# Performance work log

Hardware: AMD Instinct MI355X
Metric: run time of the kernel (lower is better)

Reference implementation:

```python
import jax, jax.numpy as jnp
import numpy as np

N, E = 100000, 1000000
IN_F, HID, OUT, K = 64, 64, 32, 3


def setup_inputs() -> dict:
    key = jax.random.key(0)
    ks = jax.random.split(key, 8)
    s = 0.05
    return {
        "features": jax.random.normal(ks[0], (N, IN_F), dtype=jnp.float32),
        "src": jax.random.randint(ks[1], (E,), 0, N),
        "dst": jax.random.randint(ks[2], (E,), 0, N),
        "n_nodes": N,
        "W1": jax.random.normal(ks[3], (K * IN_F, HID), jnp.float32) * s,
        "b1": jnp.zeros((HID,), jnp.float32),
        "W2": jax.random.normal(ks[4], (K * HID, HID), jnp.float32) * s,
        "b2": jnp.zeros((HID,), jnp.float32),
        "Wm1": jax.random.normal(ks[5], (HID, HID), jnp.float32) * s,
        "bm1": jnp.zeros((HID,), jnp.float32),
        "Wm2": jax.random.normal(ks[6], (HID, OUT), jnp.float32) * s,
        "bm2": jnp.zeros((OUT,), jnp.float32),
    }


def _cheb_conv(x, src, dst, dinv, W, b, n_nodes, k=K):
    # DGL ChebConv with lambda_max = 2 (re_norm = 2/lambda_max = 1).
    def prop(h):  # D^{-1/2} A D^{-1/2} h via edge gather/scatter
        m = (h * dinv)[src]                                   # [E, F]
        agg = jax.ops.segment_sum(m, dst, num_segments=n_nodes)
        return agg * dinv

    X0 = x
    Xs = [X0]
    X1 = -prop(X0)                 # -re_norm*L h + (re_norm-1)*X0, re_norm=1
    Xs.append(X1)
    for _ in range(2, k):
        Xi = -2.0 * prop(X1) - X0  # Chebyshev recursion
        Xs.append(Xi)
        X0, X1 = X1, Xi
    return jnp.concatenate(Xs, axis=1) @ W + b  # Linear(k*F_in -> F_out)


def reference(features, src, dst, n_nodes, W1, b1, W2, b2, Wm1, bm1, Wm2, bm2):
    deg = jax.ops.segment_sum(
        jnp.ones((src.shape[0],), dtype=features.dtype), dst, num_segments=n_nodes
    )
    dinv = (jnp.clip(deg, 1.0, None) ** -0.5)[:, None]  # in-degree^{-1/2}
    x = jax.nn.relu(_cheb_conv(features, src, dst, dinv, W1, b1, n_nodes))
    x = jax.nn.relu(_cheb_conv(x, src, dst, dinv, W2, b2, n_nodes))
    return jax.nn.relu(x @ Wm1 + bm1) @ Wm2 + bm2
```

## Files before the change

kernel.cpp:

```cpp
#include <hip/hip_runtime.h>


typedef unsigned short ushort_t;
typedef __attribute__((ext_vector_type(8))) short v8s;
typedef __attribute__((ext_vector_type(4))) float v4f;

__device__ inline ushort_t f2bf(float f) {
    unsigned u = __float_as_uint(f);
    return (ushort_t)((u + 0x7FFFu + ((u >> 16) & 1u)) >> 16);
}
__device__ inline float bf2f(ushort_t h) {
    return __uint_as_float(((unsigned)h) << 16);
}

#define BSH 9
#define BSZ (1 << BSH)
#define CHUNK 4096

__global__ void k_wprep(const float* __restrict__ W1, const float* __restrict__ W2,
                        const float* __restrict__ Wm1, const float* __restrict__ Wm2,
                        ushort_t* __restrict__ W1t, ushort_t* __restrict__ W2t,
                        ushort_t* __restrict__ Wm1t, ushort_t* __restrict__ Wm2t,
                        int* __restrict__ gbase, int NB) {
    int i = blockIdx.x * 256 + threadIdx.x;
    if (i < 12288) { int k = i >> 6, n = i & 63; W1t[n * 192 + k] = f2bf(W1[i]); return; }
    i -= 12288;
    if (i < 12288) { int k = i >> 6, n = i & 63; W2t[n * 192 + k] = f2bf(W2[i]); return; }
    i -= 12288;
    if (i < 4096) { int k = i >> 6, n = i & 63; Wm1t[n * 64 + k] = f2bf(Wm1[i]); return; }
    i -= 4096;
    if (i < 2048) { int k = i >> 5, n = i & 31; Wm2t[n * 64 + k] = f2bf(Wm2[i]); return; }
    i -= 2048;
    if (i < NB) gbase[i] = 0;
}


__global__ __launch_bounds__(256) void k_bhist(const int* __restrict__ dst,
                                               int* __restrict__ gbase, int E, int NB) {
    __shared__ int h[1024];
    for (int i = threadIdx.x; i < NB; i += 256) h[i] = 0;
    __syncthreads();
    for (int i = blockIdx.x * blockDim.x + threadIdx.x; i < E; i += gridDim.x * blockDim.x)
        atomicAdd(&h[dst[i] >> BSH], 1);
    __syncthreads();
    for (int i = threadIdx.x; i < NB; i += 256)
        if (h[i]) atomicAdd(&gbase[i], h[i]);
}

__global__ void k_bscan(int* __restrict__ gbase, int* __restrict__ gcur, int NB) {
    __shared__ int sh[1024];
    int t = threadIdx.x;
    int v = (t < NB) ? gbase[t] : 0;
    sh[t] = v;
    __syncthreads();
    for (int off = 1; off < 1024; off <<= 1) {
        int u = 0;
        if (t >= off) u = sh[t - off];
        __syncthreads();
        sh[t] += u;
        __syncthreads();
    }
    if (t < NB) {
        int excl = sh[t] - v;
        gbase[t] = excl;
        gcur[t] = excl;
    }
}

__global__ __launch_bounds__(256) void k_bucket2(
    const int* __restrict__ src, const int* __restrict__ dst,
    int* __restrict__ gcur, int2* __restrict__ eb, int E, int NB) {
    __shared__ int ls[CHUNK];
    __shared__ int ld[CHUNK];
    __shared__ int hist[1024];
    __shared__ int bbase[1024];
    int t = threadIdx.x;
    int base = blockIdx.x * CHUNK;
    int count = E - base;
    if (count > CHUNK) count = CHUNK;
    for (int i = t; i < NB; i += 256) hist[i] = 0;
    __syncthreads();
    for (int i = t; i < count; i += 256) {
        int s = src[base + i];
        int d = dst[base + i];
        ls[i] = s;
        ld[i] = d;
        atomicAdd(&hist[d >> BSH], 1);
    }
    __syncthreads();
    for (int b = t; b < NB; b += 256) {
        int c = hist[b];
        bbase[b] = c ? atomicAdd(&gcur[b], c) : 0;
        hist[b] = 0;
    }
    __syncthreads();
    for (int i = t; i < count; i += 256) {
        int d = ld[i];
        int b = d >> BSH;
        int off = atomicAdd(&hist[b], 1);
        eb[bbase[b] + off] = make_int2(ls[i], d);
    }
}

__global__ __launch_bounds__(256) void k_local(
    const int2* __restrict__ eb, const int* __restrict__ gbase,
    int* __restrict__ col, int* __restrict__ row_ptr,
    float* __restrict__ dinv, int N, int E, int NB) {
    __shared__ int cnt[BSZ];
    __shared__ int tsum[256];
    int t = threadIdx.x;
    int b = blockIdx.x;
    int d0 = b << BSH;
    cnt[2 * t] = 0;
    cnt[2 * t + 1] = 0;
    __syncthreads();
    int beg = gbase[b];
    int end = (b + 1 < NB) ? gbase[b + 1] : E;
    for (int i = beg + t; i < end; i += 256)
        atomicAdd(&cnt[eb[i].y - d0], 1);
    __syncthreads();
    int c0 = cnt[2 * t], c1 = cnt[2 * t + 1];
    int mysum = c0 + c1;
    tsum[t] = mysum;
    __syncthreads();
    for (int off = 1; off < 256; off <<= 1) {
        int u = 0;
        if (t >= off) u = tsum[t - off];
        __syncthreads();
        tsum[t] += u;
        __syncthreads();
    }
    int rbase = beg + tsum[t] - mysum;
    int d = d0 + 2 * t;
    if (d < N) {
        row_ptr[d] = rbase;
        dinv[d] = rsqrtf(fmaxf((float)c0, 1.0f));
    }
    if (d + 1 < N) {
        row_ptr[d + 1] = rbase + c0;
        dinv[d + 1] = rsqrtf(fmaxf((float)c1, 1.0f));
    }
    cnt[2 * t] = rbase;
    cnt[2 * t + 1] = rbase + c0;
    __syncthreads();
    for (int i = beg + t; i < end; i += 256) {
        int2 e = eb[i];
        int p = atomicAdd(&cnt[e.y - d0], 1);
        col[p] = e.x;
    }
    if (b == NB - 1 && t == 0) row_ptr[N] = E;
}

__global__ void k_tobf16(const float4* __restrict__ X, const float* __restrict__ dinv,
                         ushort4* __restrict__ Y, int n4) {
    int i = blockIdx.x * blockDim.x + threadIdx.x;
    if (i < n4) {
        float s = dinv[i >> 4];
        float4 v = X[i];
        ushort4 o;
        o.x = f2bf(v.x * s); o.y = f2bf(v.y * s); o.z = f2bf(v.z * s); o.w = f2bf(v.w * s);
        Y[i] = o;
    }
}

template <int MODE>
__global__ __launch_bounds__(256) void k_prop(
    const ushort_t* __restrict__ Xb, const int* __restrict__ rp,
    const int* __restrict__ col, const float* __restrict__ dinv,
    const ushort_t* __restrict__ X0b, ushort_t* __restrict__ OUTB, int N) {
    int wid = (blockIdx.x * blockDim.x + threadIdx.x) >> 6;
    int lane = threadIdx.x & 63;
    if (wid >= N) return;
    int g = lane >> 4;
    int fl = (lane & 15) * 4;
    int beg = rp[wid], end = rp[wid + 1];
    float4 a0 = make_float4(0.f, 0.f, 0.f, 0.f);
    float4 a1 = make_float4(0.f, 0.f, 0.f, 0.f);
    int e = beg + g;
    for (; e + 4 < end; e += 8) {
        int s0 = col[e], s1 = col[e + 4];
        ushort4 u0 = *(const ushort4*)&Xb[(size_t)s0 * 64 + fl];
        ushort4 u1 = *(const ushort4*)&Xb[(size_t)s1 * 64 + fl];
        a0.x += bf2f(u0.x); a0.y += bf2f(u0.y); a0.z += bf2f(u0.z); a0.w += bf2f(u0.w);
        a1.x += bf2f(u1.x); a1.y += bf2f(u1.y); a1.z += bf2f(u1.z); a1.w += bf2f(u1.w);
    }
    if (e < end) {
        int s0 = col[e];
        ushort4 u0 = *(const ushort4*)&Xb[(size_t)s0 * 64 + fl];
        a0.x += bf2f(u0.x); a0.y += bf2f(u0.y); a0.z += bf2f(u0.z); a0.w += bf2f(u0.w);
    }
    float4 acc;
    acc.x = a0.x + a1.x;
    acc.y = a0.y + a1.y;
    acc.z = a0.z + a1.z;
    acc.w = a0.w + a1.w;
    acc.x += __shfl_xor(acc.x, 16);
    acc.y += __shfl_xor(acc.y, 16);
    acc.z += __shfl_xor(acc.z, 16);
    acc.w += __shfl_xor(acc.w, 16);
    acc.x += __shfl_xor(acc.x, 32);
    acc.y += __shfl_xor(acc.y, 32);
    acc.z += __shfl_xor(acc.z, 32);
    acc.w += __shfl_xor(acc.w, 32);
    if (g == 0) {
        float di = dinv[wid];
        ushort4 ob;
        if (MODE == 1) {
            float m = -di * di;
            ob.x = f2bf(m * acc.x);
            ob.y = f2bf(m * acc.y);
            ob.z = f2bf(m * acc.z);
            ob.w = f2bf(m * acc.w);
        } else {
            ushort4 x0u = *(const ushort4*)&X0b[(size_t)wid * 64 + fl];
            float m = -2.0f * di;
            float rd = 1.0f / di;
            ob.x = f2bf(fmaf(m, acc.x, -rd * bf2f(x0u.x)));
            ob.y = f2bf(fmaf(m, acc.y, -rd * bf2f(x0u.y)));
            ob.z = f2bf(fmaf(m, acc.z, -rd * bf2f(x0u.z)));
            ob.w = f2bf(fmaf(m, acc.w, -rd * bf2f(x0u.w)));
        }
        *(ushort4*)&OUTB[(size_t)wid * 64 + fl] = ob;
    }
}

template <bool SCALE_OUT>
__global__ __launch_bounds__(256, 6) void k_cheb_mfma(
    const ushort_t* __restrict__ X0, const ushort_t* __restrict__ X1,
    const ushort_t* __restrict__ X2, const float* __restrict__ dinv,
    const ushort_t* __restrict__ Wt, const float* __restrict__ b,
    ushort_t* __restrict__ Yb, int N) {
    int wave = threadIdx.x >> 6, lane = threadIdx.x & 63;
    int n16 = lane & 15, q = lane >> 4;
    int node0 = blockIdx.x * 64;
    int arow = node0 + wave * 16 + n16;
    const ushort_t* Xc[3] = {X0, X1, X2};

    v8s av[6];
#pragma unroll
    for (int ks = 0; ks < 6; ks++) {
        int c = ks >> 1;
        int kk = (ks & 1) * 32 + q * 8;
        av[ks] = (v8s){0, 0, 0, 0, 0, 0, 0, 0};
        if (arow < N) av[ks] = *(const v8s*)&Xc[c][(size_t)arow * 64 + kk];
    }

    v4f acc_s[4], acc_u[4];
#pragma unroll
    for (int t = 0; t < 4; t++) {
        acc_s[t] = (v4f){0.f, 0.f, 0.f, 0.f};
        acc_u[t] = (v4f){0.f, 0.f, 0.f, 0.f};
    }
#pragma unroll
    for (int ks = 0; ks < 6; ks++) {
        int c = ks >> 1;
#pragma unroll
        for (int t = 0; t < 4; t++) {
            v8s bv = *(const v8s*)&Wt[(size_t)(t * 16 + n16) * 192 + ks * 32 + q * 8];
            if (c < 2)
                acc_s[t] = __builtin_amdgcn_mfma_f32_16x16x32_bf16(av[ks], bv, acc_s[t], 0, 0, 0);
            else
                acc_u[t] = __builtin_amdgcn_mfma_f32_16x16x32_bf16(av[ks], bv, acc_u[t], 0, 0, 0);
        }
    }
    int rbase = node0 + wave * 16 + q * 4;
#pragma unroll
    for (int r = 0; r < 4; r++) {
        int row = rbase + r;
        if (row < N) {
            float dv = dinv[row];
            float rd = 1.0f / dv;
            float s = SCALE_OUT ? dv : 1.0f;
#pragma unroll
            for (int t = 0; t < 4; t++) {
                float y = fmaf(rd, acc_s[t][r], acc_u[t][r]) + b[t * 16 + n16];
                y = fmaxf(y, 0.0f);
                Yb[(size_t)row * 64 + t * 16 + n16] = f2bf(s * y);
            }
        }
    }
}

__global__ __launch_bounds__(256, 6) void k_cheb_mlp(
    const ushort_t* __restrict__ X0, const ushort_t* __restrict__ X1,
    const ushort_t* __restrict__ X2, const float* __restrict__ dinv,
    const ushort_t* __restrict__ Wt, const float* __restrict__ b,
    const ushort_t* __restrict__ Wm1t, const float* __restrict__ bm1,
    const ushort_t* __restrict__ Wm2t, const float* __restrict__ bm2,
    float* __restrict__ out, int N) {
    __shared__ ushort_t Hs0[64][76];
    __shared__ ushort_t Hs1[64][76];
    int wave = threadIdx.x >> 6, lane = threadIdx.x & 63;
    int n16 = lane & 15, q = lane >> 4;
    int node0 = blockIdx.x * 64;
    int arow = node0 + wave * 16 + n16;
    const ushort_t* Xc[3] = {X0, X1, X2};

    v8s av[6];
#pragma unroll
    for (int ks = 0; ks < 6; ks++) {
        int c = ks >> 1;
        int kk = (ks & 1) * 32 + q * 8;
        av[ks] = (v8s){0, 0, 0, 0, 0, 0, 0, 0};
        if (arow < N) av[ks] = *(const v8s*)&Xc[c][(size_t)arow * 64 + kk];
    }

    v4f acc_s[4], acc_u[4];
#pragma unroll
    for (int t = 0; t < 4; t++) {
        acc_s[t] = (v4f){0.f, 0.f, 0.f, 0.f};
        acc_u[t] = (v4f){0.f, 0.f, 0.f, 0.f};
    }
#pragma unroll
    for (int ks = 0; ks < 6; ks++) {
        int c = ks >> 1;
#pragma unroll
        for (int t = 0; t < 4; t++) {
            v8s bv = *(const v8s*)&Wt[(size_t)(t * 16 + n16) * 192 + ks * 32 + q * 8];
            if (c < 2)
                acc_s[t] = __builtin_amdgcn_mfma_f32_16x16x32_bf16(av[ks], bv, acc_s[t], 0, 0, 0);
            else
                acc_u[t] = __builtin_amdgcn_mfma_f32_16x16x32_bf16(av[ks], bv, acc_u[t], 0, 0, 0);
        }
    }
    int lr = wave * 16 + q * 4;
    int rbase = node0 + lr;
#pragma unroll
    for (int r = 0; r < 4; r++) {
        int row = rbase + r;
        if (row < N) {
            float dv = dinv[row];
            float rd = 1.0f / dv;
#pragma unroll
            for (int t = 0; t < 4; t++) {
                float y = fmaf(rd, acc_s[t][r], acc_u[t][r]) + b[t * 16 + n16];
                Hs0[lr + r][t * 16 + n16] = f2bf(fmaxf(y, 0.0f));
            }
        } else {
#pragma unroll
            for (int t = 0; t < 4; t++) Hs0[lr + r][t * 16 + n16] = 0;
        }
    }
    __syncthreads();

    v4f acc[4];
#pragma unroll
    for (int t = 0; t < 4; t++) acc[t] = (v4f){0.f, 0.f, 0.f, 0.f};
#pragma unroll
    for (int ks = 0; ks < 2; ks++) {
        v8s av1 = *(const v8s*)&Hs0[wave * 16 + n16][ks * 32 + q * 8];
#pragma unroll
        for (int t = 0; t < 4; t++) {
            v8s bv = *(const v8s*)&Wm1t[(size_t)(t * 16 + n16) * 64 + ks * 32 + q * 8];
            acc[t] = __builtin_amdgcn_mfma_f32_16x16x32_bf16(av1, bv, acc[t], 0, 0, 0);
        }
    }
#pragma unroll
    for (int r = 0; r < 4; r++)
#pragma unroll
        for (int t = 0; t < 4; t++) {
            float y = acc[t][r] + bm1[t * 16 + n16];
            Hs1[lr + r][t * 16 + n16] = f2bf(fmaxf(y, 0.0f));
        }
    __syncthreads();

    v4f a2[2];
    a2[0] = (v4f){0.f, 0.f, 0.f, 0.f};
    a2[1] = (v4f){0.f, 0.f, 0.f, 0.f};
#pragma unroll
    for (int ks = 0; ks < 2; ks++) {
        v8s av2 = *(const v8s*)&Hs1[wave * 16 + n16][ks * 32 + q * 8];
#pragma unroll
        for (int t = 0; t < 2; t++) {
            v8s bv = *(const v8s*)&Wm2t[(size_t)(t * 16 + n16) * 64 + ks * 32 + q * 8];
            a2[t] = __builtin_amdgcn_mfma_f32_16x16x32_bf16(av2, bv, a2[t], 0, 0, 0);
        }
    }
#pragma unroll
    for (int r = 0; r < 4; r++) {
        int row = rbase + r;
        if (row < N) {
#pragma unroll
            for (int t = 0; t < 2; t++)
                out[(size_t)row * 32 + t * 16 + n16] = a2[t][r] + bm2[t * 16 + n16];
        }
    }
}

extern "C" void kernel_launch(void* const* d_in, const int* in_sizes, int n_in,
                              void* d_out, int out_size, void* d_ws, size_t ws_size,
                              hipStream_t stream) {
    const float* features = (const float*)d_in[0];
    const int* src = (const int*)d_in[1];
    const int* dst = (const int*)d_in[2];
    const float* W1 = (const float*)d_in[4];
    const float* b1 = (const float*)d_in[5];
    const float* W2 = (const float*)d_in[6];
    const float* b2 = (const float*)d_in[7];
    const float* Wm1 = (const float*)d_in[8];
    const float* bm1 = (const float*)d_in[9];
    const float* Wm2 = (const float*)d_in[10];
    const float* bm2 = (const float*)d_in[11];
    float* out = (float*)d_out;

    int N = in_sizes[0] / 64;
    int E = in_sizes[1];
    int NB = (N + BSZ - 1) >> BSH;

    float* ws = (float*)d_ws;
    float* dinv = ws;
    int* row_ptr = (int*)(dinv + N);
    int* gbase = row_ptr + (N + 1);
    int* gcur = gbase + 1024;
    int* col = gcur + 1024;
    int2* eb = (int2*)(((uintptr_t)(col + E) + 7) & ~(uintptr_t)7);
    ushort_t* Fb  = (ushort_t*)(eb + E);
    ushort_t* X1b = Fb  + (size_t)N * 64;
    ushort_t* X2b = X1b + (size_t)N * 64;
    ushort_t* H1b = X2b + (size_t)N * 64;
    ushort_t* W1t = H1b + (size_t)N * 64;
    ushort_t* W2t = W1t + 64 * 192;
    ushort_t* Wm1t = W2t + 64 * 192;
    ushort_t* Wm2t = Wm1t + 64 * 64;

    int pblk = (N * 64 + 255) / 256;
    int gblk = (N + 63) / 64;
    int n4 = N * 16;
    int cblk = (n4 + 255) / 256;
    int bblk = (E + CHUNK - 1) / CHUNK;

    k_wprep<<<(30720 + 1024 + 255) / 256, 256, 0, stream>>>(
        W1, W2, Wm1, Wm2, W1t, W2t, Wm1t, Wm2t, gbase, NB);

    k_bhist<<<512, 256, 0, stream>>>(dst, gbase, E, NB);
    k_bscan<<<1, 1024, 0, stream>>>(gbase, gcur, NB);
    k_bucket2<<<bblk, 256, 0, stream>>>(src, dst, gcur, eb, E, NB);
    k_local<<<NB, 256, 0, stream>>>(eb, gbase, col, row_ptr, dinv, N, E, NB);

    k_tobf16<<<cblk, 256, 0, stream>>>((const float4*)features, dinv, (ushort4*)Fb, n4);

    k_prop<1><<<pblk, 256, 0, stream>>>(Fb, row_ptr, col, dinv, nullptr, X1b, N);
    k_prop<2><<<pblk, 256, 0, stream>>>(X1b, row_ptr, col, dinv, Fb, X2b, N);
    k_cheb_mfma<true><<<gblk, 256, 0, stream>>>(Fb, X1b, X2b, dinv, W1t, b1, H1b, N);

    k_prop<1><<<pblk, 256, 0, stream>>>(H1b, row_ptr, col, dinv, nullptr, X1b, N);
    k_prop<2><<<pblk, 256, 0, stream>>>(X1b, row_ptr, col, dinv, H1b, X2b, N);
    k_cheb_mlp<<<gblk, 256, 0, stream>>>(H1b, X1b, X2b, dinv, W2t, b2,
                                         Wm1t, bm1, Wm2t, bm2, out, N);
}
```

Measured before the change: 386.7 us.

## Fuse bucket scan into histogram kernel and stage Chebyshev inputs through LDS

The separate single-block scan kernel is removed. The last histogram block to finish, found with an atomic done counter and thread fences, now performs the exclusive scan over bucket counts, which saves one kernel launch. Both Chebyshev MFMA kernels now load their 64-row X0/X1/X2 tiles into shared memory with coalesced 16-byte loads and read the MFMA operands from there, with occupancy hints lowered from 6 to 4. The in-block scan only handles up to 256 buckets, and the tile loads drop the N bounds check, so the last block reads past the end of each buffer into adjacent workspace.

Measured after the change: 402.5 us. +4.1%, slower.

```diff
diff --git a/kernel.cpp b/kernel.cpp
--- a/kernel.cpp
+++ b/kernel.cpp
@@ -21,7 +21,7 @@
                         const float* __restrict__ Wm1, const float* __restrict__ Wm2,
                         ushort_t* __restrict__ W1t, ushort_t* __restrict__ W2t,
                         ushort_t* __restrict__ Wm1t, ushort_t* __restrict__ Wm2t,
-                        int* __restrict__ gbase, int NB) {
+                        int* __restrict__ gbase, int* __restrict__ done, int NB) {
     int i = blockIdx.x * 256 + threadIdx.x;
     if (i < 12288) { int k = i >> 6, n = i & 63; W1t[n * 192 + k] = f2bf(W1[i]); return; }
     i -= 12288;
@@ -32,12 +32,15 @@
     if (i < 2048) { int k = i >> 5, n = i & 31; Wm2t[n * 64 + k] = f2bf(Wm2[i]); return; }
     i -= 2048;
     if (i < NB) gbase[i] = 0;
-}
-
+    if (i == NB) *done = 0;
+}
 
 __global__ __launch_bounds__(256) void k_bhist(const int* __restrict__ dst,
-                                               int* __restrict__ gbase, int E, int NB) {
+                                               int* __restrict__ gbase,
+                                               int* __restrict__ gcur,
+                                               int* __restrict__ done, int E, int NB) {
     __shared__ int h[1024];
+    __shared__ int isLast;
     for (int i = threadIdx.x; i < NB; i += 256) h[i] = 0;
     __syncthreads();
     for (int i = blockIdx.x * blockDim.x + threadIdx.x; i < E; i += gridDim.x * blockDim.x)
@@ -45,25 +48,27 @@
     __syncthreads();
     for (int i = threadIdx.x; i < NB; i += 256)
         if (h[i]) atomicAdd(&gbase[i], h[i]);
-}
-
-__global__ void k_bscan(int* __restrict__ gbase, int* __restrict__ gcur, int NB) {
-    __shared__ int sh[1024];
-    int t = threadIdx.x;
-    int v = (t < NB) ? gbase[t] : 0;
-    sh[t] = v;
-    __syncthreads();
-    for (int off = 1; off < 1024; off <<= 1) {
-        int u = 0;
-        if (t >= off) u = sh[t - off];
+    __threadfence();
+    __syncthreads();
+    if (threadIdx.x == 0) isLast = (atomicAdd(done, 1) == (int)gridDim.x - 1);
+    __syncthreads();
+    if (isLast) {
+        __threadfence();
+        int t = threadIdx.x;
+        int v = (t < NB) ? gbase[t] : 0;
+        h[t] = v;
         __syncthreads();
-        sh[t] += u;
-        __syncthreads();
-    }
-    if (t < NB) {
-        int excl = sh[t] - v;
-        gbase[t] = excl;
-        gcur[t] = excl;
+        for (int off = 1; off < 256; off <<= 1) {
+            int u = (t >= off) ? h[t - off] : 0;
+            __syncthreads();
+            h[t] += u;
+            __syncthreads();
+        }
+        if (t < NB) {
+            int excl = h[t] - v;
+            gbase[t] = excl;
+            gcur[t] = excl;
+        }
     }
 }
 
@@ -225,25 +230,34 @@
 }
 
 template <bool SCALE_OUT>
-__global__ __launch_bounds__(256, 6) void k_cheb_mfma(
+__global__ __launch_bounds__(256, 4) void k_cheb_mfma(
     const ushort_t* __restrict__ X0, const ushort_t* __restrict__ X1,
     const ushort_t* __restrict__ X2, const float* __restrict__ dinv,
     const ushort_t* __restrict__ Wt, const float* __restrict__ b,
     ushort_t* __restrict__ Yb, int N) {
-    int wave = threadIdx.x >> 6, lane = threadIdx.x & 63;
+    __shared__ ushort_t XA[3][64][72];
+    int tid = threadIdx.x;
+    int node0 = blockIdx.x * 64;
+    const ushort_t* Xc[3] = {X0, X1, X2};
+#pragma unroll
+    for (int c = 0; c < 3; c++) {
+#pragma unroll
+        for (int p = 0; p < 2; p++) {
+            int s = p * 2048 + tid * 8;
+            int row = s >> 6, cc = s & 63;
+            v8s v = *(const v8s*)&Xc[c][((size_t)(node0 + row)) * 64 + cc];
+            *(v8s*)&XA[c][row][cc] = v;
+        }
+    }
+    __syncthreads();
+
+    int wave = tid >> 6, lane = tid & 63;
     int n16 = lane & 15, q = lane >> 4;
-    int node0 = blockIdx.x * 64;
-    int arow = node0 + wave * 16 + n16;
-    const ushort_t* Xc[3] = {X0, X1, X2};
-
+    int lrow = wave * 16 + n16;
     v8s av[6];
 #pragma unroll
-    for (int ks = 0; ks < 6; ks++) {
-        int c = ks >> 1;
-        int kk = (ks & 1) * 32 + q * 8;
-        av[ks] = (v8s){0, 0, 0, 0, 0, 0, 0, 0};
-        if (arow < N) av[ks] = *(const v8s*)&Xc[c][(size_t)arow * 64 + kk];
-    }
+    for (int ks = 0; ks < 6; ks++)
+        av[ks] = *(const v8s*)&XA[ks >> 1][lrow][(ks & 1) * 32 + q * 8];
 
     v4f acc_s[4], acc_u[4];
 #pragma unroll
@@ -281,29 +295,40 @@
     }
 }
 
-__global__ __launch_bounds__(256, 6) void k_cheb_mlp(
+__global__ __launch_bounds__(256, 4) void k_cheb_mlp(
     const ushort_t* __restrict__ X0, const ushort_t* __restrict__ X1,
     const ushort_t* __restrict__ X2, const float* __restrict__ dinv,
     const ushort_t* __restrict__ Wt, const float* __restrict__ b,
     const ushort_t* __restrict__ Wm1t, const float* __restrict__ bm1,
     const ushort_t* __restrict__ Wm2t, const float* __restrict__ bm2,
     float* __restrict__ out, int N) {
-    __shared__ ushort_t Hs0[64][76];
-    __shared__ ushort_t Hs1[64][76];
-    int wave = threadIdx.x >> 6, lane = threadIdx.x & 63;
+    __shared__ ushort_t smem[3 * 64 * 72];
+    ushort_t (*XA)[64][72] = (ushort_t(*)[64][72])smem;
+    ushort_t (*Hs0)[76] = (ushort_t(*)[76])smem;
+    ushort_t (*Hs1)[76] = (ushort_t(*)[76])(smem + 64 * 76);
+    int tid = threadIdx.x;
+    int node0 = blockIdx.x * 64;
+    const ushort_t* Xc[3] = {X0, X1, X2};
+#pragma unroll
+    for (int c = 0; c < 3; c++) {
+#pragma unroll
+        for (int p = 0; p < 2; p++) {
+            int s = p * 2048 + tid * 8;
+            int row = s >> 6, cc = s & 63;
+            v8s v = *(const v8s*)&Xc[c][((size_t)(node0 + row)) * 64 + cc];
+            *(v8s*)&XA[c][row][cc] = v;
+        }
+    }
+    __syncthreads();
+
+    int wave = tid >> 6, lane = tid & 63;
     int n16 = lane & 15, q = lane >> 4;
-    int node0 = blockIdx.x * 64;
-    int arow = node0 + wave * 16 + n16;
-    const ushort_t* Xc[3] = {X0, X1, X2};
-
+    int lrow = wave * 16 + n16;
     v8s av[6];
 #pragma unroll
-    for (int ks = 0; ks < 6; ks++) {
-        int c = ks >> 1;
-        int kk = (ks & 1) * 32 + q * 8;
-        av[ks] = (v8s){0, 0, 0, 0, 0, 0, 0, 0};
-        if (arow < N) av[ks] = *(const v8s*)&Xc[c][(size_t)arow * 64 + kk];
-    }
+    for (int ks = 0; ks < 6; ks++)
+        av[ks] = *(const v8s*)&XA[ks >> 1][lrow][(ks & 1) * 32 + q * 8];
+    __syncthreads();
 
     v4f acc_s[4], acc_u[4];
 #pragma unroll
@@ -412,7 +437,8 @@
     int* row_ptr = (int*)(dinv + N);
     int* gbase = row_ptr + (N + 1);
     int* gcur = gbase + 1024;
-    int* col = gcur + 1024;
+    int* done = gcur + 1024;
+    int* col = done + 16;
     int2* eb = (int2*)(((uintptr_t)(col + E) + 7) & ~(uintptr_t)7);
     ushort_t* Fb  = (ushort_t*)(eb + E);
     ushort_t* X1b = Fb  + (size_t)N * 64;
@@ -430,10 +456,9 @@
     int bblk = (E + CHUNK - 1) / CHUNK;
 
     k_wprep<<<(30720 + 1024 + 255) / 256, 256, 0, stream>>>(
-        W1, W2, Wm1, Wm2, W1t, W2t, Wm1t, Wm2t, gbase, NB);
-
-    k_bhist<<<512, 256, 0, stream>>>(dst, gbase, E, NB);
-    k_bscan<<<1, 1024, 0, stream>>>(gbase, gcur, NB);
+        W1, W2, Wm1, Wm2, W1t, W2t, Wm1t, Wm2t, gbase, done, NB);
+
+    k_bhist<<<512, 256, 0, stream>>>(dst, gbase, gcur, done, E, NB);
     k_bucket2<<<bblk, 256, 0, stream>>>(src, dst, gcur, eb, E, NB);
     k_local<<<NB, 256, 0, stream>>>(eb, gbase, col, row_ptr, dinv, N, E, NB);
 
```
